# Kernel tuning notes

Measured on AMD Instinct MI355X. Metric: run time of the kernel, lower is better.

## Reference

```python
import jax, jax.numpy as jnp
import numpy as np

N = 100000      # nodes
E = 1600000     # edges (before self loops)
H = 64          # hidden per head (heads=1)
CLASSES = 4
NEG = 0.2       # GATv2 leaky relu slope


def _glorot(key, shape):
    lim = (6.0 / (shape[0] + shape[1])) ** 0.5
    return jax.random.uniform(key, shape, jnp.float32, -lim, lim)


def setup_inputs() -> dict:
    key = jax.random.key(0)
    ks = jax.random.split(key, 40)
    inp = {}
    inp['x'] = jax.random.normal(ks[0], (N, 6), jnp.float32)
    inp['edge_index'] = jax.random.randint(ks[1], (2, E), 0, N, dtype=jnp.int64)
    inp['edge_attr'] = jax.random.normal(ks[2], (E, 6), jnp.float32)
    i = 3
    for l, din in ((1, 6), (2, H), (3, H)):
        inp[f'wl{l}'] = _glorot(ks[i], (din, H)); i += 1
        inp[f'bl{l}'] = jnp.zeros((H,), jnp.float32)
        inp[f'wr{l}'] = _glorot(ks[i], (din, H)); i += 1
        inp[f'br{l}'] = jnp.zeros((H,), jnp.float32)
        inp[f'we{l}'] = _glorot(ks[i], (6, H)); i += 1
        inp[f'att{l}'] = _glorot(ks[i], (H, 1))[:, 0]; i += 1
        inp[f'bo{l}'] = jnp.zeros((H,), jnp.float32)
    inp['wlin'] = _glorot(ks[i], (H, 32)); i += 1
    inp['blin'] = jnp.zeros((32,), jnp.float32)
    inp['wout'] = _glorot(ks[i], (32, CLASSES)); i += 1
    inp['bout'] = jnp.zeros((CLASSES,), jnp.float32)
    return inp


def _add_self_loops(src, dst, ea):
    # PyG add_self_loops(fill_value='mean'): loop attr = mean of incoming edge_attr per node
    cnt = jax.ops.segment_sum(jnp.ones((ea.shape[0],), jnp.float32), dst, num_segments=N)
    loop = jax.ops.segment_sum(ea, dst, num_segments=N) / jnp.maximum(cnt, 1.0)[:, None]
    ar = jnp.arange(N, dtype=src.dtype)
    return (jnp.concatenate([src, ar]), jnp.concatenate([dst, ar]),
            jnp.concatenate([ea, loop], axis=0))


def _gatv2(x, src, dst, ea, wl, bl, wr, br, we, att, bo):
    xl = x @ wl + bl                      # [N,H] source transform
    xr = x @ wr + br                      # [N,H] target transform
    xe = ea @ we                          # [E',H] edge transform (no bias)
    m = xl[src] + xr[dst] + xe            # [E',H]
    e = jax.nn.leaky_relu(m, NEG) @ att   # [E'] attention logits
    emax = jax.ops.segment_max(e, dst, num_segments=N)   # every node has a self loop
    ex = jnp.exp(e - emax[dst])
    den = jax.ops.segment_sum(ex, dst, num_segments=N)
    alpha = ex / (den[dst] + 1e-16)
    out = jax.ops.segment_sum(alpha[:, None] * xl[src], dst, num_segments=N)
    return out + bo


def reference(x, edge_index, edge_attr,
              wl1, bl1, wr1, br1, we1, att1, bo1,
              wl2, bl2, wr2, br2, we2, att2, bo2,
              wl3, bl3, wr3, br3, we3, att3, bo3,
              wlin, blin, wout, bout):
    src, dst, ea = _add_self_loops(edge_index[0], edge_index[1], edge_attr)
    h = jax.nn.relu(_gatv2(x, src, dst, ea, wl1, bl1, wr1, br1, we1, att1, bo1))
    h = jax.nn.relu(_gatv2(h, src, dst, ea, wl2, bl2, wr2, br2, we2, att2, bo2))
    h = jax.nn.relu(_gatv2(h, src, dst, ea, wl3, bl3, wr3, br3, we3, att3, bo3))
    h = jax.nn.relu(h @ wlin + blin)
    return h @ wout + bout
```

## Files before the change

### kernel.cpp

```cpp
#include <hip/hip_runtime.h>
#include <hip/hip_bf16.h>
#include <math.h>

#define NN 100000
#define NE 1600000
#define NEP 1700000
#define HD 64
#define NEGS 0.2f

typedef float f2 __attribute__((ext_vector_type(2)));
typedef float f4 __attribute__((ext_vector_type(4)));

__device__ __forceinline__ f2 sp2(float v) { return (f2){v, v}; }
__device__ __forceinline__ f4 sp4(float v) { return (f4){v, v, v, v}; }
__device__ __forceinline__ f2 ffma2(f2 a, f2 b, f2 c) {
#if __has_builtin(__builtin_elementwise_fma)
  return __builtin_elementwise_fma(a, b, c);
#else
  return a * b + c;
#endif
}
__device__ __forceinline__ f4 ffma4(f4 a, f4 b, f4 c) {
#if __has_builtin(__builtin_elementwise_fma)
  return __builtin_elementwise_fma(a, b, c);
#else
  return a * b + c;
#endif
}
__device__ __forceinline__ f2 fmax2(f2 a, f2 b) {
#if __has_builtin(__builtin_elementwise_max)
  return __builtin_elementwise_max(a, b);
#else
  f2 r; r.x = fmaxf(a.x, b.x); r.y = fmaxf(a.y, b.y); return r;
#endif
}
__device__ __forceinline__ f4 fmax4(f4 a, f4 b) {
#if __has_builtin(__builtin_elementwise_max)
  return __builtin_elementwise_max(a, b);
#else
  f4 r; r.x = fmaxf(a.x, b.x); r.y = fmaxf(a.y, b.y);
  r.z = fmaxf(a.z, b.z); r.w = fmaxf(a.w, b.w); return r;
#endif
}


__global__ void k_init_cnt(int* __restrict__ cnt, int* __restrict__ hist,
                           int* __restrict__ cursor2) {
  int i = blockIdx.x * 256 + threadIdx.x;
  if (i < NN) cnt[i] = 1;
  if (blockIdx.x == 0) {
    if (threadIdx.x < 64) hist[threadIdx.x] = 0;
    else if (threadIdx.x < 128) cursor2[threadIdx.x - 64] = 0;
  }
}

__global__ void k_count_rank(const int* __restrict__ dst, int* __restrict__ cnt,
                             int* __restrict__ rank) {
  int base = (blockIdx.x * 256 + threadIdx.x) * 4;
  if (base >= NE) return;
  int4 dv = *(const int4*)(dst + base);
  int4 rv;
  rv.x = atomicAdd(&cnt[dv.x], 1);
  rv.y = atomicAdd(&cnt[dv.y], 1);
  rv.z = atomicAdd(&cnt[dv.z], 1);
  rv.w = atomicAdd(&cnt[dv.w], 1);
  *(int4*)(rank + base) = rv;
}

__global__ void k_scan_a(const int* __restrict__ cnt, int* __restrict__ rp,
                         int* __restrict__ bsum, int* __restrict__ hist) {
  __shared__ int tmp[1024];
  __shared__ int lh[64];
  int t = threadIdx.x, b = blockIdx.x;
  int i = b * 1024 + t;
  int v = (i < NN) ? cnt[i] : 0;
  tmp[t] = v;
  if (t < 64) lh[t] = 0;
  __syncthreads();
  if (i < NN) atomicAdd(&lh[v < 63 ? v : 63], 1);
  for (int off = 1; off < 1024; off <<= 1) {
    int a = (t >= off) ? tmp[t - off] : 0;
    __syncthreads(); tmp[t] += a; __syncthreads();
  }
  if (i < NN) rp[i] = tmp[t] - v;
  if (t == 1023) bsum[b] = tmp[t];
  if (t < 64) { int h = lh[t]; if (h) atomicAdd(&hist[t], h); }
}

__global__ void k_scan_b(const int* __restrict__ bsum, int* __restrict__ boff, int nb,
                         const int* __restrict__ hist, int* __restrict__ cursor2) {
  __shared__ int tmp[1024];
  int t = threadIdx.x;
  int v = (t < nb) ? bsum[t] : 0;
  tmp[t] = v; __syncthreads();
  for (int off = 1; off < 1024; off <<= 1) {
    int a = (t >= off) ? tmp[t - off] : 0;
    __syncthreads(); tmp[t] += a; __syncthreads();
  }
  if (t < nb) boff[t] = tmp[t] - v;
  if (t < 64) {
    int h = hist[t];
    int s = h;
#pragma unroll
    for (int off = 1; off < 64; off <<= 1) {
      int u = __shfl_up(s, off);
      if (t >= off) s += u;
    }
    cursor2[t] = s - h;
  }
}

__global__ void k_scan_c(int* __restrict__ rp, const int* __restrict__ boff,
                         const int* __restrict__ deg,
                         int* __restrict__ cursor2, int* __restrict__ order) {
  __shared__ int lh[64];
  __shared__ int lbase[64];
  int t = threadIdx.x, b = blockIdx.x;
  int i = b * 1024 + t;
  if (t < 64) lh[t] = 0;
  __syncthreads();
  int bin = 0, lr = 0;
  if (i < NN) {
    int d = deg[i];
    bin = d < 63 ? d : 63;
    lr = atomicAdd(&lh[bin], 1);
    rp[i] = rp[i] + boff[b];
  }
  __syncthreads();
  if (t < 64) {
    int h = lh[t];
    lbase[t] = h ? atomicAdd(&cursor2[t], h) : 0;
  }
  __syncthreads();
  if (i < NN) order[lbase[bin] + lr] = i;
  if (i == 0) rp[NN] = NEP;
}

__global__ void __launch_bounds__(256) k_scatter3(
    const int* __restrict__ src, const int* __restrict__ dst,
    const int* __restrict__ rank, const float* __restrict__ ea,
    const int* __restrict__ rp, float* __restrict__ rec) {
  int base = (blockIdx.x * 256 + threadIdx.x) * 4;
  if (base >= NE) return;
  int4 sv = *(const int4*)(src + base);
  int4 dv = *(const int4*)(dst + base);
  int4 rv = *(const int4*)(rank + base);
  const float4* e4 = (const float4*)(ea + (size_t)base * 6);
  float4 e0 = e4[0], e1 = e4[1], e2 = e4[2], e3 = e4[3], e4v = e4[4], e5 = e4[5];
  int d[4] = {dv.x, dv.y, dv.z, dv.w};
  int rk[4] = {rv.x, rv.y, rv.z, rv.w};
  int s[4] = {sv.x, sv.y, sv.z, sv.w};
  int p[4];
#pragma unroll
  for (int k = 0; k < 4; ++k) p[k] = rp[d[k]] + rk[k];
  float a[24] = {e0.x, e0.y, e0.z, e0.w, e1.x, e1.y, e1.z, e1.w,
                 e2.x, e2.y, e2.z, e2.w, e3.x, e3.y, e3.z, e3.w,
                 e4v.x, e4v.y, e4v.z, e4v.w, e5.x, e5.y, e5.z, e5.w};
#pragma unroll
  for (int k = 0; k < 4; ++k) {
    float* r = rec + (size_t)p[k] * 8;
    *(float4*)r       = make_float4(__int_as_float(s[k]),
                                    a[6 * k + 0], a[6 * k + 1], a[6 * k + 2]);
    *(float4*)(r + 4) = make_float4(a[6 * k + 3], a[6 * k + 4], a[6 * k + 5], 0.f);
  }
}

__global__ void __launch_bounds__(256) k_lamean2(const int* __restrict__ rp,
                                                 float* __restrict__ rec) {
  int tid = threadIdx.x;
  int q = tid & 15;
  int n = (blockIdx.x * 256 + tid) >> 4;
  if (n >= NN) return;
  int p0 = rp[n], p1 = rp[n + 1];
  float s0 = 0, s1 = 0, s2 = 0, s3 = 0, s4 = 0, s5 = 0;
  for (int p = p0 + 1 + q; p < p1; p += 16) {
    const float* r = rec + (size_t)p * 8;
    float4 r0 = *(const float4*)r;
    float4 r1 = *(const float4*)(r + 4);
    s0 += r0.y; s1 += r0.z; s2 += r0.w;
    s3 += r1.x; s4 += r1.y; s5 += r1.z;
  }
#pragma unroll
  for (int off = 1; off < 16; off <<= 1) {
    s0 += __shfl_xor(s0, off); s1 += __shfl_xor(s1, off);
    s2 += __shfl_xor(s2, off); s3 += __shfl_xor(s3, off);
    s4 += __shfl_xor(s4, off); s5 += __shfl_xor(s5, off);
  }
  if (q == 0) {
    int c = p1 - p0 - 1;
    float inv = c > 0 ? 1.0f / (float)c : 0.0f;
    float* r = rec + (size_t)p0 * 8;
    *(float4*)r       = make_float4(__int_as_float(n), s0 * inv, s1 * inv, s2 * inv);
    *(float4*)(r + 4) = make_float4(s3 * inv, s4 * inv, s5 * inv, 0.f);
  }
}

template <int DIN>
__global__ void __launch_bounds__(256) k_xform(
    const float* __restrict__ x,
    const float* __restrict__ wl, const float* __restrict__ bl,
    const float* __restrict__ wr, const float* __restrict__ br,
    float* __restrict__ xl, float* __restrict__ xr) {
  int tid = threadIdx.x;
  int lane = tid & 63, wid = tid >> 6;
  int h = lane;
  float wlr[DIN], wrr[DIN];
#pragma unroll
  for (int k = 0; k < DIN; ++k) { wlr[k] = wl[k * 64 + h]; wrr[k] = wr[k * 64 + h]; }
  float blv = bl[h], brv = br[h];
  int stride = gridDim.x * 4;
  for (int n = blockIdx.x * 4 + wid; n < NN; n += stride) {
    float xv = (lane < DIN) ? x[(size_t)n * DIN + lane] : 0.0f;
    float aL = blv, aR = brv;
#pragma unroll
    for (int k = 0; k < DIN; ++k) {
      float xk = __shfl(xv, k);
      aL = fmaf(xk, wlr[k], aL);
      aR = fmaf(xk, wrr[k], aR);
    }
    xl[(size_t)n * 64 + h] = aL;
    xr[(size_t)n * 64 + h] = aR;
  }
}

__global__ void __launch_bounds__(256) k_fused(
    const float* __restrict__ xl, const float* __restrict__ xr,
    const float* __restrict__ rec,
    const int* __restrict__ rp, const int* __restrict__ order,
    const float* __restrict__ we, const float* __restrict__ att,
    const float* __restrict__ bo, float* __restrict__ hout) {
  int tid = threadIdx.x;
  int lane = tid & 63;
  int q = lane & 15;
  int c0 = q * 4;
  f2 w0a, w0b, w1a, w1b, w2a, w2b, w3a, w3b, w4a, w4b, w5a, w5b;
  w0a = *(const f2*)(we + 0 * 64 + c0); w0b = *(const f2*)(we + 0 * 64 + c0 + 2);
  w1a = *(const f2*)(we + 1 * 64 + c0); w1b = *(const f2*)(we + 1 * 64 + c0 + 2);
  w2a = *(const f2*)(we + 2 * 64 + c0); w2b = *(const f2*)(we + 2 * 64 + c0 + 2);
  w3a = *(const f2*)(we + 3 * 64 + c0); w3b = *(const f2*)(we + 3 * 64 + c0 + 2);
  w4a = *(const f2*)(we + 4 * 64 + c0); w4b = *(const f2*)(we + 4 * 64 + c0 + 2);
  w5a = *(const f2*)(we + 5 * 64 + c0); w5b = *(const f2*)(we + 5 * 64 + c0 + 2);
  f2 ata = *(const f2*)(att + c0) * 1.44269504f;
  f2 atb = *(const f2*)(att + c0 + 2) * 1.44269504f;
  f2 boa = *(const f2*)(bo + c0);
  f2 bob = *(const f2*)(bo + c0 + 2);
  int gw = (blockIdx.x * 256 + tid) >> 6;
  int slot = gw * 4 + (lane >> 4);
  int n = (slot < NN) ? order[NN - 1 - slot] : -1;
  int p0 = 0, p1 = 0;
  f2 xra = (f2){0, 0}, xrb2 = (f2){0, 0};
  if (n >= 0) {
    p0 = rp[n]; p1 = rp[n + 1];
    const f4 t = *(const f4*)(xr + (size_t)n * 64 + c0);
    xra = (f2){t.x, t.y}; xrb2 = (f2){t.z, t.w};
  }
  float m = -INFINITY, den = 0.0f;
  f2 acca = (f2){0, 0}, accb = (f2){0, 0};
  int p = p0;
  for (; p + 2 <= p1; p += 2) {
    const f4* ra = (const f4*)(rec + (size_t)p * 8);
    f4 qa0 = ra[0], qa1 = ra[1], qb0 = ra[2], qb1 = ra[3];
    int sA = __float_as_int(qa0.x), sB = __float_as_int(qb0.x);
    f4 xA = *(const f4*)(xl + (size_t)sA * 64 + c0);
    f4 xB = *(const f4*)(xl + (size_t)sB * 64 + c0);
    f2 xAa = (f2){xA.x, xA.y}, xAb = (f2){xA.z, xA.w};
    f2 xBa = (f2){xB.x, xB.y}, xBb = (f2){xB.z, xB.w};
    f2 tA = xAa + xra;
    tA = ffma2(sp2(qa0.y), w0a, tA); tA = ffma2(sp2(qa0.z), w1a, tA);
    tA = ffma2(sp2(qa0.w), w2a, tA); tA = ffma2(sp2(qa1.x), w3a, tA);
    tA = ffma2(sp2(qa1.y), w4a, tA); tA = ffma2(sp2(qa1.z), w5a, tA);
    f2 pav = fmax2(tA, sp2(0.2f) * tA) * ata;
    f2 uA = xAb + xrb2;
    uA = ffma2(sp2(qa0.y), w0b, uA); uA = ffma2(sp2(qa0.z), w1b, uA);
    uA = ffma2(sp2(qa0.w), w2b, uA); uA = ffma2(sp2(qa1.x), w3b, uA);
    uA = ffma2(sp2(qa1.y), w4b, uA); uA = ffma2(sp2(qa1.z), w5b, uA);
    pav = ffma2(fmax2(uA, sp2(0.2f) * uA), atb, pav);
    f2 tB = xBa + xra;
    tB = ffma2(sp2(qb0.y), w0a, tB); tB = ffma2(sp2(qb0.z), w1a, tB);
    tB = ffma2(sp2(qb0.w), w2a, tB); tB = ffma2(sp2(qb1.x), w3a, tB);
    tB = ffma2(sp2(qb1.y), w4a, tB); tB = ffma2(sp2(qb1.z), w5a, tB);
    f2 pbv = fmax2(tB, sp2(0.2f) * tB) * ata;
    f2 uB = xBb + xrb2;
    uB = ffma2(sp2(qb0.y), w0b, uB); uB = ffma2(sp2(qb0.z), w1b, uB);
    uB = ffma2(sp2(qb0.w), w2b, uB); uB = ffma2(sp2(qb1.x), w3b, uB);
    uB = ffma2(sp2(qb1.y), w4b, uB); uB = ffma2(sp2(qb1.z), w5b, uB);
    pbv = ffma2(fmax2(uB, sp2(0.2f) * uB), atb, pbv);
    float pa = pav.x + pav.y;
    float pb = pbv.x + pbv.y;
    pa += __shfl_xor(pa, 1); pb += __shfl_xor(pb, 1);
    pa += __shfl_xor(pa, 2); pb += __shfl_xor(pb, 2);
    pa += __shfl_xor(pa, 4); pb += __shfl_xor(pb, 4);
    pa += __shfl_xor(pa, 8); pb += __shfl_xor(pb, 8);
    float nm = fmaxf(m, fmaxf(pa, pb));
    float sc = exp2f(m - nm);
    float eA = exp2f(pa - nm);
    float eB = exp2f(pb - nm);
    m = nm;
    den = fmaf(den, sc, eA + eB);
    acca = ffma2(acca, sp2(sc), ffma2(sp2(eA), xAa, sp2(eB) * xBa));
    accb = ffma2(accb, sp2(sc), ffma2(sp2(eA), xAb, sp2(eB) * xBb));
  }
  if (p < p1) {
    const f4* ra = (const f4*)(rec + (size_t)p * 8);
    f4 r0 = ra[0], r1 = ra[1];
    int s = __float_as_int(r0.x);
    f4 xt = *(const f4*)(xl + (size_t)s * 64 + c0);
    f2 xa = (f2){xt.x, xt.y}, xb = (f2){xt.z, xt.w};
    f2 t = xa + xra;
    t = ffma2(sp2(r0.y), w0a, t); t = ffma2(sp2(r0.z), w1a, t);
    t = ffma2(sp2(r0.w), w2a, t); t = ffma2(sp2(r1.x), w3a, t);
    t = ffma2(sp2(r1.y), w4a, t); t = ffma2(sp2(r1.z), w5a, t);
    f2 pv = fmax2(t, sp2(0.2f) * t) * ata;
    f2 u = xb + xrb2;
    u = ffma2(sp2(r0.y), w0b, u); u = ffma2(sp2(r0.z), w1b, u);
    u = ffma2(sp2(r0.w), w2b, u); u = ffma2(sp2(r1.x), w3b, u);
    u = ffma2(sp2(r1.y), w4b, u); u = ffma2(sp2(r1.z), w5b, u);
    pv = ffma2(fmax2(u, sp2(0.2f) * u), atb, pv);
    float part = pv.x + pv.y;
    part += __shfl_xor(part, 1);
    part += __shfl_xor(part, 2);
    part += __shfl_xor(part, 4);
    part += __shfl_xor(part, 8);
    float nm = fmaxf(m, part);
    float sc = exp2f(m - nm);
    float ex = exp2f(part - nm);
    m = nm;
    den = fmaf(den, sc, ex);
    acca = ffma2(acca, sp2(sc), sp2(ex) * xa);
    accb = ffma2(accb, sp2(sc), sp2(ex) * xb);
  }
  if (n >= 0) {
    float inv = 1.0f / (den + 1e-16f);
    f2 oa = ffma2(acca, sp2(inv), boa);
    f2 ob = ffma2(accb, sp2(inv), bob);
    oa = fmax2(oa, (f2){0, 0});
    ob = fmax2(ob, (f2){0, 0});
    f4 o = (f4){oa.x, oa.y, ob.x, ob.y};
    *(f4*)(hout + (size_t)n * 64 + c0) = o;
  }
}

__global__ void __launch_bounds__(256) k_mlp2(
    const float* __restrict__ hin,
    const float* __restrict__ wlin, const float* __restrict__ blin,
    const float* __restrict__ wout, const float* __restrict__ bout,
    float* __restrict__ out) {
  __shared__ float wl_s[64 * 32];
  __shared__ float bl_s[32];
  __shared__ float wo_s[32 * 4];
  __shared__ float bo_s[4];
  int tid = threadIdx.x;
#pragma unroll
  for (int i = 0; i < 8; ++i) wl_s[tid + i * 256] = wlin[tid + i * 256];
  if (tid < 128) wo_s[tid] = wout[tid];
  if (tid < 32) bl_s[tid] = blin[tid];
  if (tid >= 32 && tid < 36) bo_s[tid - 32] = bout[tid - 32];
  __syncthreads();
  int n = blockIdx.x * 256 + tid;
  if (n >= NN) return;
  const f4* hp = (const f4*)(hin + (size_t)n * 64);
  f4 h[16];
#pragma unroll
  for (int i = 0; i < 16; ++i) h[i] = hp[i];
  f4 acc[8];
#pragma unroll
  for (int j4 = 0; j4 < 8; ++j4) acc[j4] = *(const f4*)(bl_s + j4 * 4);
#pragma unroll
  for (int k = 0; k < 64; ++k) {
    float hk = ((const float*)h)[k];
    const f4* wrow = (const f4*)(wl_s + k * 32);
#pragma unroll
    for (int j4 = 0; j4 < 8; ++j4)
      acc[j4] = ffma4(sp4(hk), wrow[j4], acc[j4]);
  }
  f4 o4 = *(const f4*)(bo_s);
#pragma unroll
  for (int j4 = 0; j4 < 8; ++j4) {
    f4 hid = fmax4(acc[j4], sp4(0.0f));
    const f4* wo = (const f4*)(wo_s + j4 * 16);
    o4 = ffma4(sp4(hid.x), wo[0], o4);
    o4 = ffma4(sp4(hid.y), wo[1], o4);
    o4 = ffma4(sp4(hid.z), wo[2], o4);
    o4 = ffma4(sp4(hid.w), wo[3], o4);
  }
  *(f4*)(out + (size_t)n * 4) = o4;
}


extern "C" void kernel_launch(void* const* d_in, const int* in_sizes, int n_in,
                              void* d_out, int out_size, void* d_ws, size_t ws_size,
                              hipStream_t stream) {
  const float* x  = (const float*)d_in[0];
  const int*   ei = (const int*)d_in[1];
  const float* ea = (const float*)d_in[2];
  const int* src = ei;
  const int* dst = ei + NE;

  const float *wl[3], *bl[3], *wrm[3], *br[3], *wem[3], *attv[3], *bov[3];
  for (int l = 0; l < 3; ++l) {
    int b = 3 + l * 7;
    wl[l]  = (const float*)d_in[b + 0];
    bl[l]  = (const float*)d_in[b + 1];
    wrm[l] = (const float*)d_in[b + 2];
    br[l]  = (const float*)d_in[b + 3];
    wem[l] = (const float*)d_in[b + 4];
    attv[l]= (const float*)d_in[b + 5];
    bov[l] = (const float*)d_in[b + 6];
  }
  const float* wlin = (const float*)d_in[24];
  const float* blin = (const float*)d_in[25];
  const float* wout = (const float*)d_in[26];
  const float* bout = (const float*)d_in[27];
  float* outp = (float*)d_out;

  char* w = (char*)d_ws;
  size_t off = 0;
  auto carve = [&](size_t bytes) -> void* {
    void* p = w + off;
    off += (bytes + 255) & ~(size_t)255;
    return p;
  };
  int*   cnt  = (int*)carve((size_t)NN * 4);
  int*   rp   = (int*)carve((size_t)(NN + 1) * 4);
  int*   bsum = (int*)carve(1024 * 4);
  int*   boff = (int*)carve(1024 * 4);
  int*   hist = (int*)carve(64 * 4);
  int*   cur2 = (int*)carve(64 * 4);
  int*   order= (int*)carve((size_t)NN * 4);
  int*   rank = (int*)carve((size_t)NE * 4);
  float* rec  = (float*)carve((size_t)NEP * 32);
  float* xlb  = (float*)carve((size_t)NN * 64 * 4);
  float* xrb  = (float*)carve((size_t)NN * 64 * 4);
  float* hA   = (float*)carve((size_t)NN * 64 * 4);
  float* hB   = (float*)carve((size_t)NN * 64 * 4);
  (void)ws_size; (void)n_in; (void)in_sizes; (void)out_size;

  const int SCAN_NB = (NN + 1023) / 1024;
  const int FUSE_NB = (NN + 15) / 16;
  const int CR_NB   = (NE / 4 + 255) / 256;

  hipLaunchKernelGGL(k_init_cnt, dim3((NN + 255) / 256), dim3(256), 0, stream,
                     cnt, hist, cur2);
  hipLaunchKernelGGL(k_count_rank, dim3(CR_NB), dim3(256), 0, stream, dst, cnt, rank);
  hipLaunchKernelGGL(k_scan_a, dim3(SCAN_NB), dim3(1024), 0, stream, cnt, rp, bsum, hist);
  hipLaunchKernelGGL(k_scan_b, dim3(1), dim3(1024), 0, stream, bsum, boff, SCAN_NB,
                     hist, cur2);
  hipLaunchKernelGGL(k_scan_c, dim3(SCAN_NB), dim3(1024), 0, stream, rp, boff, cnt,
                     cur2, order);
  hipLaunchKernelGGL(k_scatter3, dim3(CR_NB), dim3(256), 0, stream,
                     src, dst, rank, ea, rp, rec);
  hipLaunchKernelGGL(k_lamean2, dim3((NN + 15) / 16), dim3(256), 0, stream, rp, rec);

  hipLaunchKernelGGL((k_xform<6>), dim3(1024), dim3(256), 0, stream,
                     x, wl[0], bl[0], wrm[0], br[0], xlb, xrb);
  hipLaunchKernelGGL(k_fused, dim3(FUSE_NB), dim3(256), 0, stream,
                     xlb, xrb, rec, rp, order, wem[0], attv[0], bov[0], hA);
  hipLaunchKernelGGL((k_xform<64>), dim3(2048), dim3(256), 0, stream,
                     hA, wl[1], bl[1], wrm[1], br[1], xlb, xrb);
  hipLaunchKernelGGL(k_fused, dim3(FUSE_NB), dim3(256), 0, stream,
                     xlb, xrb, rec, rp, order, wem[1], attv[1], bov[1], hB);
  hipLaunchKernelGGL((k_xform<64>), dim3(2048), dim3(256), 0, stream,
                     hB, wl[2], bl[2], wrm[2], br[2], xlb, xrb);
  hipLaunchKernelGGL(k_fused, dim3(FUSE_NB), dim3(256), 0, stream,
                     xlb, xrb, rec, rp, order, wem[2], attv[2], bov[2], hA);
  hipLaunchKernelGGL(k_mlp2, dim3((NN + 255) / 256), dim3(256), 0, stream,
                     hA, wlin, blin, wout, bout, outp);
}
```

Baseline: 539.7 us.

## Restructure node transform to one node per thread with LDS-staged weights

The xl/xr transform kernel is rewritten so each thread owns a whole node: it loads the node's 64 input features into registers, reads both weight matrices from shared memory (broadcast reads), and accumulates 64 outputs per matrix with packed f4 FMAs. The old version used one wavefront per node with shuffles to broadcast each input element. This is meant to remove the per-element shuffle cost and make better use of the FMA units. In exchange it needs many registers per thread (64 inputs plus 16 f4 accumulators), which may lower occupancy, and the per-thread row loads and stores are strided across lanes and poorly coalesced.

Result: no change. 544.8 us (+0.9%).

```diff
diff --git a/kernel.cpp b/kernel.cpp
--- a/kernel.cpp
+++ b/kernel.cpp
@@ -196,31 +196,58 @@
 }
 
 template <int DIN>
-__global__ void __launch_bounds__(256) k_xform(
+__global__ void __launch_bounds__(256) k_xform2(
     const float* __restrict__ x,
     const float* __restrict__ wl, const float* __restrict__ bl,
     const float* __restrict__ wr, const float* __restrict__ br,
     float* __restrict__ xl, float* __restrict__ xr) {
+  __shared__ f4 w_s[DIN * 32];
+  __shared__ f4 b_s[32];
   int tid = threadIdx.x;
-  int lane = tid & 63, wid = tid >> 6;
-  int h = lane;
-  float wlr[DIN], wrr[DIN];
-#pragma unroll
-  for (int k = 0; k < DIN; ++k) { wlr[k] = wl[k * 64 + h]; wrr[k] = wr[k * 64 + h]; }
-  float blv = bl[h], brv = br[h];
-  int stride = gridDim.x * 4;
-  for (int n = blockIdx.x * 4 + wid; n < NN; n += stride) {
-    float xv = (lane < DIN) ? x[(size_t)n * DIN + lane] : 0.0f;
-    float aL = blv, aR = brv;
-#pragma unroll
-    for (int k = 0; k < DIN; ++k) {
-      float xk = __shfl(xv, k);
-      aL = fmaf(xk, wlr[k], aL);
-      aR = fmaf(xk, wrr[k], aR);
-    }
-    xl[(size_t)n * 64 + h] = aL;
-    xr[(size_t)n * 64 + h] = aR;
-  }
+  for (int idx = tid; idx < DIN * 16; idx += 256) {
+    int k = idx >> 4, j = idx & 15;
+    w_s[k * 32 + j]      = *(const f4*)(wl + k * 64 + j * 4);
+    w_s[k * 32 + 16 + j] = *(const f4*)(wr + k * 64 + j * 4);
+  }
+  if (tid < 16) b_s[tid] = *(const f4*)(bl + tid * 4);
+  else if (tid < 32) b_s[tid] = *(const f4*)(br + (tid - 16) * 4);
+  __syncthreads();
+  int n = blockIdx.x * 256 + tid;
+  if (n >= NN) return;
+  float h[DIN];
+  if (DIN == 64) {
+    const f4* xp = (const f4*)(x + (size_t)n * 64);
+#pragma unroll
+    for (int i = 0; i < 16; ++i) *(f4*)(h + i * 4) = xp[i];
+  } else {
+#pragma unroll
+    for (int i = 0; i < DIN; ++i) h[i] = x[(size_t)n * DIN + i];
+  }
+  f4 acc[16];
+#pragma unroll
+  for (int j = 0; j < 16; ++j) acc[j] = b_s[j];
+#pragma unroll
+  for (int k = 0; k < DIN; ++k) {
+    f4 hk = sp4(h[k]);
+#pragma unroll
+    for (int j = 0; j < 16; ++j)
+      acc[j] = ffma4(hk, w_s[k * 32 + j], acc[j]);
+  }
+  f4* lo = (f4*)(xl + (size_t)n * 64);
+#pragma unroll
+  for (int j = 0; j < 16; ++j) lo[j] = acc[j];
+#pragma unroll
+  for (int j = 0; j < 16; ++j) acc[j] = b_s[16 + j];
+#pragma unroll
+  for (int k = 0; k < DIN; ++k) {
+    f4 hk = sp4(h[k]);
+#pragma unroll
+    for (int j = 0; j < 16; ++j)
+      acc[j] = ffma4(hk, w_s[k * 32 + 16 + j], acc[j]);
+  }
+  f4* ro = (f4*)(xr + (size_t)n * 64);
+#pragma unroll
+  for (int j = 0; j < 16; ++j) ro[j] = acc[j];
 }
 
 __global__ void __launch_bounds__(256) k_fused(
@@ -438,6 +465,7 @@
   const int SCAN_NB = (NN + 1023) / 1024;
   const int FUSE_NB = (NN + 15) / 16;
   const int CR_NB   = (NE / 4 + 255) / 256;
+  const int XF_NB   = (NN + 255) / 256;
 
   hipLaunchKernelGGL(k_init_cnt, dim3((NN + 255) / 256), dim3(256), 0, stream,
                      cnt, hist, cur2);
@@ -451,15 +479,15 @@
                      src, dst, rank, ea, rp, rec);
   hipLaunchKernelGGL(k_lamean2, dim3((NN + 15) / 16), dim3(256), 0, stream, rp, rec);
 
-  hipLaunchKernelGGL((k_xform<6>), dim3(1024), dim3(256), 0, stream,
+  hipLaunchKernelGGL((k_xform2<6>), dim3(XF_NB), dim3(256), 0, stream,
                      x, wl[0], bl[0], wrm[0], br[0], xlb, xrb);
   hipLaunchKernelGGL(k_fused, dim3(FUSE_NB), dim3(256), 0, stream,
                      xlb, xrb, rec, rp, order, wem[0], attv[0], bov[0], hA);
-  hipLaunchKernelGGL((k_xform<64>), dim3(2048), dim3(256), 0, stream,
+  hipLaunchKernelGGL((k_xform2<64>), dim3(XF_NB), dim3(256), 0, stream,
                      hA, wl[1], bl[1], wrm[1], br[1], xlb, xrb);
   hipLaunchKernelGGL(k_fused, dim3(FUSE_NB), dim3(256), 0, stream,
                      xlb, xrb, rec, rp, order, wem[1], attv[1], bov[1], hB);
-  hipLaunchKernelGGL((k_xform<64>), dim3(2048), dim3(256), 0, stream,
+  hipLaunchKernelGGL((k_xform2<64>), dim3(XF_NB), dim3(256), 0, stream,
                      hB, wl[2], bl[2], wrm[2], br[2], xlb, xrb);
   hipLaunchKernelGGL(k_fused, dim3(FUSE_NB), dim3(256), 0, stream,
                      xlb, xrb, rec, rp, order, wem[2], attv[2], bov[2], hA);
```
